# Kernel tuning notes

Hardware: AMD Instinct MI355X
Metric: run time of the kernel (lower is better)

The kernel has to match this reference:

```python
import jax, jax.numpy as jnp
import numpy as np

N, E = 50000, 1600000
D_IN, D_HID, D_OUT = 256, 256, 128  # 2*output_dim = 256, output_dim = 128


def glorot(key, shape):
    fan_in, fan_out = shape
    limit = np.sqrt(6.0 / (fan_in + fan_out)).astype(np.float32)
    return jax.random.uniform(key, shape, jnp.float32, -limit, limit)


def setup_inputs() -> dict:
    key = jax.random.key(0)
    k0, k1, k2, k3 = jax.random.split(key, 4)
    x = jax.random.normal(k0, (N, D_IN), jnp.float32)
    edge_index = jax.random.randint(k1, (2, E), 0, N, jnp.int32)
    W1 = glorot(k2, (D_IN, D_HID))
    b1 = jnp.zeros((D_HID,), jnp.float32)
    W2 = glorot(k3, (D_HID, D_OUT))
    b2 = jnp.zeros((D_OUT,), jnp.float32)
    return {"x": x, "edge_index": edge_index, "W1": W1, "b1": b1, "W2": W2, "b2": b2}


def gcn_propagate(x, src, dst, num_nodes):
    """One hop of D^-1/2 (A + I) D^-1/2 @ x (PyG gcn_norm with self-loops)."""
    loops = jnp.arange(num_nodes, dtype=src.dtype)
    src_sl = jnp.concatenate([src, loops])  # [E + N]
    dst_sl = jnp.concatenate([dst, loops])
    ones = jnp.ones(src_sl.shape, x.dtype)
    deg = jax.ops.segment_sum(ones, dst_sl, num_segments=num_nodes)  # >= 1 (self-loop)
    dinv = jax.lax.rsqrt(jnp.maximum(deg, 1e-12))
    norm = dinv[src_sl] * dinv[dst_sl]  # [E + N]
    msgs = x[src_sl] * norm[:, None]    # gather + scale, [E+N, D]
    return jax.ops.segment_sum(msgs, dst_sl, num_segments=num_nodes)


def reference(x, edge_index, W1, b1, W2, b2):
    src, dst = edge_index[0], edge_index[1]
    n = x.shape[0]
    # SGConv(K=1): propagate then linear. conv1 + ReLU
    h = jax.nn.relu(gcn_propagate(x, src, dst, n) @ W1 + b1)
    # conv2 (GAE branch)
    return gcn_propagate(h, src, dst, n) @ W2 + b2
```

## Files before the change

### kernel.cpp

```cpp
#include <hip/hip_runtime.h>

typedef short s16x8 __attribute__((ext_vector_type(8)));
typedef float f32x4 __attribute__((ext_vector_type(4)));
typedef float f32x2 __attribute__((ext_vector_type(2)));

#define TILE 2048

__device__ __forceinline__ unsigned int brne(float f) {
    unsigned int u = __float_as_uint(f);
    return (u + 0x7FFFu + ((u >> 16) & 1u)) >> 16;
}
__device__ __forceinline__ float blo(unsigned int u) { return __uint_as_float(u << 16); }
__device__ __forceinline__ float bhi(unsigned int u) { return __uint_as_float(u & 0xFFFF0000u); }

__device__ __forceinline__ unsigned int pk_bf16(float lo, float hi) {
    unsigned int r;
    asm("v_cvt_pk_bf16_f32 %0, %1, %2" : "=v"(r) : "v"(lo), "v"(hi));
    return r;
}

__device__ __forceinline__ void acc8p(f32x2* a, const uint4 u, const f32x2 w2) {
    a[0] += (f32x2){blo(u.x), bhi(u.x)} * w2;
    a[1] += (f32x2){blo(u.y), bhi(u.y)} * w2;
    a[2] += (f32x2){blo(u.z), bhi(u.z)} * w2;
    a[3] += (f32x2){blo(u.w), bhi(u.w)} * w2;
}

__device__ __forceinline__ void acc16p(f32x2* a, const uint4 u, const f32x2 w2) {
    a[0] += __builtin_amdgcn_cvt_pk_f32_fp8((int)u.x, false) * w2;
    a[1] += __builtin_amdgcn_cvt_pk_f32_fp8((int)u.x, true)  * w2;
    a[2] += __builtin_amdgcn_cvt_pk_f32_fp8((int)u.y, false) * w2;
    a[3] += __builtin_amdgcn_cvt_pk_f32_fp8((int)u.y, true)  * w2;
    a[4] += __builtin_amdgcn_cvt_pk_f32_fp8((int)u.z, false) * w2;
    a[5] += __builtin_amdgcn_cvt_pk_f32_fp8((int)u.z, true)  * w2;
    a[6] += __builtin_amdgcn_cvt_pk_f32_fp8((int)u.w, false) * w2;
    a[7] += __builtin_amdgcn_cvt_pk_f32_fp8((int)u.w, true)  * w2;
}


__global__ void k_bhist_tw(const int* __restrict__ dst, int* __restrict__ bucket_cnt,
                           int e, int nb, int nbt,
                           const float* __restrict__ W1, const float* __restrict__ W2,
                           unsigned short* __restrict__ W1t, unsigned short* __restrict__ W2t) {
    const int tid = threadIdx.x;
    if ((int)blockIdx.x >= nbt) {
        const int t = ((int)blockIdx.x - nbt) * 256 + tid;
        if (t < 65536) {
            const int k = t >> 8, nn = t & 255;
            W1t[nn * 256 + k] = (unsigned short)brne(W1[t]);
        } else {
            const int u = t - 65536;
            const int k = u >> 7, nn = u & 127;
            W2t[nn * 256 + k] = (unsigned short)brne(W2[u]);
        }
        return;
    }
    __shared__ int h[256];
    h[tid] = 0;
    __syncthreads();
    const int base = blockIdx.x * TILE + tid;
#pragma unroll
    for (int k = 0; k < 8; k++) {
        const int i = base + k * 256;
        if (i < e) atomicAdd(&h[dst[i] >> 8], 1);
    }
    __syncthreads();
    if (tid < nb && h[tid]) atomicAdd(&bucket_cnt[tid], h[tid]);
}

__global__ void k_bscan(const int* __restrict__ bucket_cnt, int* __restrict__ bucket_base,
                        int* __restrict__ bucket_cursor, int nb, int e) {
    __shared__ int sh[256];
    const int tid = threadIdx.x;
    const int v = (tid < nb) ? bucket_cnt[tid] : 0;
    int x = v;
    sh[tid] = x;
    __syncthreads();
    for (int off = 1; off < 256; off <<= 1) {
        const int t = (tid >= off) ? sh[tid - off] : 0;
        __syncthreads();
        if (tid >= off) { x += t; sh[tid] = x; }
        __syncthreads();
    }
    if (tid < nb) { bucket_base[tid] = x - v; bucket_cursor[tid] = x - v; }
    if (tid == 0) bucket_base[nb] = e;
}

__global__ void k_bscatter(const int* __restrict__ src, const int* __restrict__ dst,
                           int* __restrict__ bucket_cursor, uint2* __restrict__ eb, int e) {
    __shared__ int h[256], hbase[256], h2[256];
    const int tid = threadIdx.x;
    h[tid] = 0; h2[tid] = 0;
    __syncthreads();
    const int base = blockIdx.x * TILE + tid;
    int s[8], d[8], b[8];
    bool val[8];
#pragma unroll
    for (int k = 0; k < 8; k++) {
        const int i = base + k * 256;
        val[k] = i < e;
        if (val[k]) {
            s[k] = src[i]; d[k] = dst[i]; b[k] = d[k] >> 8;
            atomicAdd(&h[b[k]], 1);
        }
    }
    __syncthreads();
    if (h[tid]) hbase[tid] = atomicAdd(&bucket_cursor[tid], h[tid]);
    __syncthreads();
#pragma unroll
    for (int k = 0; k < 8; k++) {
        if (val[k]) {
            const int off = atomicAdd(&h2[b[k]], 1);
            eb[hbase[b[k]] + off] = make_uint2((unsigned)s[k], (unsigned)d[k]);
        }
    }
}

__global__ void k_nhist_scan(const uint2* __restrict__ eb, const int* __restrict__ bucket_base,
                             int* __restrict__ rowptr, int* __restrict__ part,
                             float* __restrict__ dinv, int n) {
    __shared__ int c[256], sh[256];
    const int tid = threadIdx.x, b = blockIdx.x;
    c[tid] = 0;
    __syncthreads();
    const int beg = bucket_base[b], end = bucket_base[b + 1];
    for (int i = beg + tid; i < end; i += 256)
        atomicAdd(&c[eb[i].y & 255], 1);
    __syncthreads();
    const int v = c[tid];
    const int node = b * 256 + tid;
    if (node < n) dinv[node] = rsqrtf((float)(v + 1));
    int x = v;
    sh[tid] = x;
    __syncthreads();
    for (int off = 1; off < 256; off <<= 1) {
        const int t = (tid >= off) ? sh[tid - off] : 0;
        __syncthreads();
        if (tid >= off) { x += t; sh[tid] = x; }
        __syncthreads();
    }
    if (node <= n) rowptr[node] = x - v;
    if (tid == 255) part[b] = x;
}

template <bool PREW>
__global__ void k_place(const uint2* __restrict__ eb, const int* __restrict__ bucket_base,
                        int* __restrict__ rowptr, const int* __restrict__ part,
                        void* __restrict__ esv, const float* __restrict__ dinv,
                        int n, int nb) {
    __shared__ int sh[256], rp[256], offs[256];
    __shared__ float sdv[256];
    const int tid = threadIdx.x, b = blockIdx.x;
    int x = (tid < nb) ? part[tid] : 0;
    sh[tid] = x;
    __syncthreads();
    for (int off = 1; off < 256; off <<= 1) {
        const int t = (tid >= off) ? sh[tid - off] : 0;
        __syncthreads();
        if (tid >= off) { x += t; sh[tid] = x; }
        __syncthreads();
    }
    const int prefix = (b > 0) ? sh[b - 1] : 0;
    const int node = b * 256 + tid;
    int rg = 0;
    if (node <= n) {
        rg = rowptr[node] + prefix;
        rowptr[node] = rg;
    }
    rp[tid] = rg;
    offs[tid] = 0;
    if (PREW) sdv[tid] = (node < n) ? dinv[node] : 0.f;
    __syncthreads();
    const int beg = bucket_base[b], end = bucket_base[b + 1];
    if (PREW) {
        int2* es2 = (int2*)esv;
        for (int i = beg + tid; i < end; i += 256) {
            const uint2 ed = eb[i];
            const int sI = (int)ed.x, d = (int)ed.y & 255;
            const float w = dinv[sI] * sdv[d];
            const int local = atomicAdd(&offs[d], 1);
            es2[rp[d] + local] = make_int2(sI, __float_as_int(w));
        }
    } else {
        int* es1 = (int*)esv;
        for (int i = beg + tid; i < end; i += 256) {
            const uint2 ed = eb[i];
            const int d = (int)ed.y & 255;
            const int local = atomicAdd(&offs[d], 1);
            es1[rp[d] + local] = (int)ed.x;
        }
    }
}

#define LP 40
template <bool AF32, bool FP8OUT>
__global__ __launch_bounds__(256) void k_gemm(const void* __restrict__ Av,
                                              const unsigned short* __restrict__ Bt,
                                              void* __restrict__ Cout,
                                              int M, int Nc) {
    __shared__ unsigned short As[128 * LP];
    __shared__ unsigned short Bs[128 * LP];

    const int tid = threadIdx.x;
    const int wave = tid >> 6, lane = tid & 63;
    const int wm = (wave >> 1) * 64, wn = (wave & 1) * 64;
    const int l15 = lane & 15, quad = lane >> 4;
    const int mBase = blockIdx.x * 128, nBase = blockIdx.y * 128;

    f32x4 acc[4][4];
#pragma unroll
    for (int i = 0; i < 4; i++)
#pragma unroll
        for (int j = 0; j < 4; j++) acc[i][j] = (f32x4){0.f, 0.f, 0.f, 0.f};

    const int r0 = tid >> 2, kc0 = tid & 3;
    int am0 = mBase + r0;      if (am0 >= M) am0 = M - 1;
    int am1 = mBase + r0 + 64; if (am1 >= M) am1 = M - 1;

    const uint4* Ap0; const uint4* Ap1; const float4* Af0; const float4* Af1;
    if (AF32) {
        Af0 = (const float4*)Av + (size_t)am0 * 64 + kc0 * 2;
        Af1 = (const float4*)Av + (size_t)am1 * 64 + kc0 * 2;
    } else {
        Ap0 = (const uint4*)Av + (size_t)am0 * 32 + kc0;
        Ap1 = (const uint4*)Av + (size_t)am1 * 32 + kc0;
    }
    const uint4* Bp0 = (const uint4*)Bt + (size_t)(nBase + r0) * 32 + kc0;
    const uint4* Bp1 = (const uint4*)Bt + (size_t)(nBase + r0 + 64) * 32 + kc0;

    for (int kt = 0; kt < 8; ++kt) {
        uint4 a0, a1;
        if (AF32) {
            const float4 l0 = Af0[kt * 8], h0 = Af0[kt * 8 + 1];
            const float4 l1 = Af1[kt * 8], h1 = Af1[kt * 8 + 1];
            a0.x = pk_bf16(l0.x, l0.y); a0.y = pk_bf16(l0.z, l0.w);
            a0.z = pk_bf16(h0.x, h0.y); a0.w = pk_bf16(h0.z, h0.w);
            a1.x = pk_bf16(l1.x, l1.y); a1.y = pk_bf16(l1.z, l1.w);
            a1.z = pk_bf16(h1.x, h1.y); a1.w = pk_bf16(h1.z, h1.w);
        } else {
            a0 = Ap0[kt * 4];
            a1 = Ap1[kt * 4];
        }
        const uint4 b0 = Bp0[kt * 4];
        const uint4 b1 = Bp1[kt * 4];
        __syncthreads();
        *(uint4*)&As[r0 * LP + kc0 * 8] = a0;
        *(uint4*)&As[(r0 + 64) * LP + kc0 * 8] = a1;
        *(uint4*)&Bs[r0 * LP + kc0 * 8] = b0;
        *(uint4*)&Bs[(r0 + 64) * LP + kc0 * 8] = b1;
        __syncthreads();

        s16x8 af[4], bf[4];
#pragma unroll
        for (int i = 0; i < 4; i++)
            af[i] = *(const s16x8*)&As[(wm + i * 16 + l15) * LP + quad * 8];
#pragma unroll
        for (int j = 0; j < 4; j++)
            bf[j] = *(const s16x8*)&Bs[(wn + j * 16 + l15) * LP + quad * 8];
#pragma unroll
        for (int i = 0; i < 4; i++)
#pragma unroll
            for (int j = 0; j < 4; j++)
                acc[i][j] = __builtin_amdgcn_mfma_f32_16x16x32_bf16(af[i], bf[j], acc[i][j], 0, 0, 0);
    }

#pragma unroll
    for (int i = 0; i < 4; i++) {
        const int rowb = mBase + wm + i * 16 + quad * 4;
#pragma unroll
        for (int j = 0; j < 4; j++) {
            const int col = nBase + wn + j * 16 + l15;
#pragma unroll
            for (int r = 0; r < 4; r += 2) {
                if (FP8OUT) {
                    const unsigned int pk = __builtin_amdgcn_cvt_pk_fp8_f32(
                        acc[i][j][r], acc[i][j][r + 1], 0, false);
                    if (rowb + r < M)
                        ((unsigned char*)Cout)[(size_t)(rowb + r) * Nc + col] =
                            (unsigned char)pk;
                    if (rowb + r + 1 < M)
                        ((unsigned char*)Cout)[(size_t)(rowb + r + 1) * Nc + col] =
                            (unsigned char)(pk >> 8);
                } else {
                    const unsigned int pk = pk_bf16(acc[i][j][r], acc[i][j][r + 1]);
                    if (rowb + r < M)
                        ((unsigned short*)Cout)[(size_t)(rowb + r) * Nc + col] =
                            (unsigned short)pk;
                    if (rowb + r + 1 < M)
                        ((unsigned short*)Cout)[(size_t)(rowb + r + 1) * Nc + col] =
                            (unsigned short)(pk >> 16);
                }
            }
        }
    }
}


template <bool PREW>
__global__ void k_prop256f8(const uint4* __restrict__ X4,
                            const int* __restrict__ rowptr,
                            const void* __restrict__ esv,
                            const float* __restrict__ dinv,
                            const float* __restrict__ bias,
                            uint4* __restrict__ Y4, int n) {
    const int wid = (int)((blockIdx.x * blockDim.x + threadIdx.x) >> 6);
    const int lane = threadIdx.x & 63;
    const int quad = lane >> 4, l16 = lane & 15;
    if (wid >= n) return;
    const float dd = dinv[wid];
    const int2* es2 = (const int2*)esv;
    const int*  es1 = (const int*)esv;
    f32x2 a[8];
#pragma unroll
    for (int k = 0; k < 8; k++) a[k] = (f32x2){0.f, 0.f};

    const int beg = rowptr[wid], end = rowptr[wid + 1];
    int j = beg + quad;

    auto EDGE = [&](int jj, int& s, float& w) {
        const bool v = jj < end;
        const int idx = v ? jj : 0;
        if (PREW) {
            const int2 p = es2[idx];
            s = p.x;
            w = v ? __int_as_float(p.y) : 0.f;
        } else {
            s = es1[idx];
            w = v ? dinv[s] * dd : 0.f;
        }
    };

    int s0, s1, s2, s3;
    float w0, w1, w2, w3;
    EDGE(j, s0, w0); EDGE(j + 4, s1, w1); EDGE(j + 8, s2, w2); EDGE(j + 12, s3, w3);

    if (quad == 0) {
        const uint4 v = X4[(size_t)wid * 16 + l16];
        acc16p(a, v, (f32x2){dd * dd, dd * dd});
    }

    while (j + 12 < end) {
        const uint4 u0 = X4[(size_t)s0 * 16 + l16];
        const uint4 u1 = X4[(size_t)s1 * 16 + l16];
        const uint4 u2 = X4[(size_t)s2 * 16 + l16];
        const uint4 u3 = X4[(size_t)s3 * 16 + l16];
        j += 16;
        int t0, t1, t2, t3;
        float x0, x1, x2, x3;
        EDGE(j, t0, x0); EDGE(j + 4, t1, x1); EDGE(j + 8, t2, x2); EDGE(j + 12, t3, x3);
        acc16p(a, u0, (f32x2){w0, w0});
        acc16p(a, u1, (f32x2){w1, w1});
        acc16p(a, u2, (f32x2){w2, w2});
        acc16p(a, u3, (f32x2){w3, w3});
        s0 = t0; s1 = t1; s2 = t2; s3 = t3;
        w0 = x0; w1 = x1; w2 = x2; w3 = x3;
    }
    {
        const uint4 u0 = X4[(size_t)s0 * 16 + l16];
        const uint4 u1 = X4[(size_t)s1 * 16 + l16];
        const uint4 u2 = X4[(size_t)s2 * 16 + l16];
        acc16p(a, u0, (f32x2){w0, w0});
        acc16p(a, u1, (f32x2){w1, w1});
        acc16p(a, u2, (f32x2){w2, w2});
    }
#pragma unroll
    for (int k = 0; k < 8; k++) {
        a[k][0] += __shfl_xor(a[k][0], 16);
        a[k][1] += __shfl_xor(a[k][1], 16);
        a[k][0] += __shfl_xor(a[k][0], 32);
        a[k][1] += __shfl_xor(a[k][1], 32);
    }
    if (quad == 0) {
        const float4* bp = (const float4*)bias + l16 * 4;
#pragma unroll
        for (int q = 0; q < 4; q++) {
            const float4 b = bp[q];
            a[2 * q][0]     = fmaxf(a[2 * q][0] + b.x, 0.f);
            a[2 * q][1]     = fmaxf(a[2 * q][1] + b.y, 0.f);
            a[2 * q + 1][0] = fmaxf(a[2 * q + 1][0] + b.z, 0.f);
            a[2 * q + 1][1] = fmaxf(a[2 * q + 1][1] + b.w, 0.f);
        }
        uint4 p0, p1;
        p0.x = pk_bf16(a[0][0], a[0][1]);
        p0.y = pk_bf16(a[1][0], a[1][1]);
        p0.z = pk_bf16(a[2][0], a[2][1]);
        p0.w = pk_bf16(a[3][0], a[3][1]);
        p1.x = pk_bf16(a[4][0], a[4][1]);
        p1.y = pk_bf16(a[5][0], a[5][1]);
        p1.z = pk_bf16(a[6][0], a[6][1]);
        p1.w = pk_bf16(a[7][0], a[7][1]);
        Y4[(size_t)wid * 32 + l16 * 2] = p0;
        Y4[(size_t)wid * 32 + l16 * 2 + 1] = p1;
    }
}

template <bool PREW>
__global__ void k_prop128b(const uint4* __restrict__ X4,
                           const int* __restrict__ rowptr,
                           const void* __restrict__ esv,
                           const float* __restrict__ dinv,
                           const float* __restrict__ bias,
                           float* __restrict__ Yout, int n) {
    const int wid = (int)((blockIdx.x * blockDim.x + threadIdx.x) >> 6);
    const int lane = threadIdx.x & 63;
    const int quad = lane >> 4, l16 = lane & 15;
    if (wid >= n) return;
    const float dd = dinv[wid];
    const int2* es2 = (const int2*)esv;
    const int*  es1 = (const int*)esv;
    f32x2 a[4];
#pragma unroll
    for (int k = 0; k < 4; k++) a[k] = (f32x2){0.f, 0.f};

    const int beg = rowptr[wid], end = rowptr[wid + 1];
    int j = beg + quad;

    auto EDGE = [&](int jj, int& s, float& w) {
        const bool v = jj < end;
        const int idx = v ? jj : 0;
        if (PREW) {
            const int2 p = es2[idx];
            s = p.x;
            w = v ? __int_as_float(p.y) : 0.f;
        } else {
            s = es1[idx];
            w = v ? dinv[s] * dd : 0.f;
        }
    };

    int s0, s1, s2, s3;
    float w0, w1, w2, w3;
    EDGE(j, s0, w0); EDGE(j + 4, s1, w1); EDGE(j + 8, s2, w2); EDGE(j + 12, s3, w3);

    if (quad == 0) {
        const uint4 v = X4[(size_t)wid * 16 + l16];
        acc8p(a, v, (f32x2){dd * dd, dd * dd});
    }

    while (j + 12 < end) {
        const uint4 u0 = X4[(size_t)s0 * 16 + l16];
        const uint4 u1 = X4[(size_t)s1 * 16 + l16];
        const uint4 u2 = X4[(size_t)s2 * 16 + l16];
        const uint4 u3 = X4[(size_t)s3 * 16 + l16];
        j += 16;
        int t0, t1, t2, t3;
        float x0, x1, x2, x3;
        EDGE(j, t0, x0); EDGE(j + 4, t1, x1); EDGE(j + 8, t2, x2); EDGE(j + 12, t3, x3);
        acc8p(a, u0, (f32x2){w0, w0});
        acc8p(a, u1, (f32x2){w1, w1});
        acc8p(a, u2, (f32x2){w2, w2});
        acc8p(a, u3, (f32x2){w3, w3});
        s0 = t0; s1 = t1; s2 = t2; s3 = t3;
        w0 = x0; w1 = x1; w2 = x2; w3 = x3;
    }
    {
        const uint4 u0 = X4[(size_t)s0 * 16 + l16];
        const uint4 u1 = X4[(size_t)s1 * 16 + l16];
        const uint4 u2 = X4[(size_t)s2 * 16 + l16];
        acc8p(a, u0, (f32x2){w0, w0});
        acc8p(a, u1, (f32x2){w1, w1});
        acc8p(a, u2, (f32x2){w2, w2});
    }
#pragma unroll
    for (int k = 0; k < 4; k++) {
        a[k][0] += __shfl_xor(a[k][0], 16);
        a[k][1] += __shfl_xor(a[k][1], 16);
        a[k][0] += __shfl_xor(a[k][0], 32);
        a[k][1] += __shfl_xor(a[k][1], 32);
    }
    if (quad == 0) {
        const float4 b0 = ((const float4*)bias)[l16 * 2];
        const float4 b1 = ((const float4*)bias)[l16 * 2 + 1];
        float4* op = (float4*)Yout + (size_t)wid * 32 + l16 * 2;
        op[0] = make_float4(a[0][0] + b0.x, a[0][1] + b0.y, a[1][0] + b0.z, a[1][1] + b0.w);
        op[1] = make_float4(a[2][0] + b1.x, a[2][1] + b1.y, a[3][0] + b1.z, a[3][1] + b1.w);
    }
}

extern "C" void kernel_launch(void* const* d_in, const int* in_sizes, int n_in,
                              void* d_out, int out_size, void* d_ws, size_t ws_size,
                              hipStream_t stream) {
    const float* x  = (const float*)d_in[0];
    const int*   ei = (const int*)d_in[1];
    const float* W1 = (const float*)d_in[2];
    const float* b1 = (const float*)d_in[3];
    const float* W2 = (const float*)d_in[4];
    const float* b2 = (const float*)d_in[5];
    float* out = (float*)d_out;

    const int n = in_sizes[0] / 256;
    const int e = in_sizes[1] / 2;
    const int* src = ei;
    const int* dst = ei + e;
    const int nb = (n + 255) >> 8;

    auto al = [](size_t v) { return (v + 511) & ~(size_t)511; };
    const size_t fixed = al(sizeof(float) * n) + al(sizeof(int) * (n + 1)) +
                         al(1024) + al(1024) + al(sizeof(int) * 257) + al(1024) +
                         al(2ull * 256 * 256) + al(2ull * 128 * 256) +
                         al((size_t)n * 256) + al(2ull * n * 256) + al(2ull * n * 128);
    const bool prew = (fixed + al(8ull * (size_t)e)) <= ws_size;

    char* wsp = (char*)d_ws;
    size_t off = 0;
    auto alloc = [&](size_t bytes) -> char* {
        char* p = wsp + off;
        off += (bytes + 511) & ~(size_t)511;
        return p;
    };
    float* dinv    = (float*)alloc(sizeof(float) * n);
    int*   rowptr  = (int*)alloc(sizeof(int) * (n + 1));
    int*   part    = (int*)alloc(1024);
    int*   bcnt    = (int*)alloc(1024);
    int*   bbase   = (int*)alloc(sizeof(int) * 257);
    int*   bcur    = (int*)alloc(1024);
    void*  es      = (void*)alloc((prew ? 8ull : 4ull) * (size_t)e);
    unsigned short* W1t = (unsigned short*)alloc(2ull * 256 * 256);
    unsigned short* W2t = (unsigned short*)alloc(2ull * 128 * 256);
    unsigned char*  T1  = (unsigned char*)alloc((size_t)n * 256);
    unsigned short* H   = (unsigned short*)alloc(2ull * n * 256);
    unsigned short* T2  = (unsigned short*)alloc(2ull * n * 128);
    uint2* eb = (uint2*)H;

    const int nb_t = (e + TILE - 1) / TILE;
    const int tw_b = (65536 + 32768) / 256;

    (void)hipMemsetAsync(bcnt, 0, sizeof(int) * 256, stream);
    k_bhist_tw<<<nb_t + tw_b, 256, 0, stream>>>(dst, bcnt, e, nb, nb_t, W1, W2, W1t, W2t);
    k_bscan<<<1, 256, 0, stream>>>(bcnt, bbase, bcur, nb, e);
    k_bscatter<<<nb_t, 256, 0, stream>>>(src, dst, bcur, eb, e);
    k_nhist_scan<<<nb, 256, 0, stream>>>(eb, bbase, rowptr, part, dinv, n);
    if (prew)
        k_place<true><<<nb, 256, 0, stream>>>(eb, bbase, rowptr, part, es, dinv, n, nb);
    else
        k_place<false><<<nb, 256, 0, stream>>>(eb, bbase, rowptr, part, es, dinv, n, nb);

    dim3 g1((n + 127) / 128, 2);
    k_gemm<true, true><<<g1, 256, 0, stream>>>(x, W1t, T1, n, 256);
    if (prew)
        k_prop256f8<true><<<(n + 3) / 4, 256, 0, stream>>>((const uint4*)T1, rowptr, es,
                                                           dinv, b1, (uint4*)H, n);
    else
        k_prop256f8<false><<<(n + 3) / 4, 256, 0, stream>>>((const uint4*)T1, rowptr, es,
                                                            dinv, b1, (uint4*)H, n);

    dim3 g2((n + 127) / 128, 1);
    k_gemm<false, false><<<g2, 256, 0, stream>>>(H, W2t, T2, n, 128);
    if (prew)
        k_prop128b<true><<<(n + 3) / 4, 256, 0, stream>>>((const uint4*)T2, rowptr, es,
                                                          dinv, b2, out, n);
    else
        k_prop128b<false><<<(n + 3) / 4, 256, 0, stream>>>((const uint4*)T2, rowptr, es,
                                                           dinv, b2, out, n);
}
```

Before: 317.1 us.

## Overlap first GEMM with graph preprocessing on a second stream, double-buffer GEMM LDS

The weight transpose and first GEMM are moved to a separate non-blocking stream, joined by events, so they run concurrently with the edge bucketing and CSR build. The bucket scan kernel is folded into the scatter kernel: every block recomputes the prefix sum from the counts, which removes one launch. The GEMM gains a double-buffered shared-memory tile so the next K-slice's global loads overlap the MFMA work on the current one. The cost is doubled LDS per GEMM block, redundant scans in every scatter block, and reliance on static stream and event state.

```diff
diff --git a/kernel.cpp b/kernel.cpp
--- a/kernel.cpp
+++ b/kernel.cpp
@@ -38,24 +38,10 @@
 }
 
 
-__global__ void k_bhist_tw(const int* __restrict__ dst, int* __restrict__ bucket_cnt,
-                           int e, int nb, int nbt,
-                           const float* __restrict__ W1, const float* __restrict__ W2,
-                           unsigned short* __restrict__ W1t, unsigned short* __restrict__ W2t) {
+__global__ void k_bhist(const int* __restrict__ dst, int* __restrict__ bucket_cnt,
+                        int e, int nb) {
+    __shared__ int h[256];
     const int tid = threadIdx.x;
-    if ((int)blockIdx.x >= nbt) {
-        const int t = ((int)blockIdx.x - nbt) * 256 + tid;
-        if (t < 65536) {
-            const int k = t >> 8, nn = t & 255;
-            W1t[nn * 256 + k] = (unsigned short)brne(W1[t]);
-        } else {
-            const int u = t - 65536;
-            const int k = u >> 7, nn = u & 127;
-            W2t[nn * 256 + k] = (unsigned short)brne(W2[u]);
-        }
-        return;
-    }
-    __shared__ int h[256];
     h[tid] = 0;
     __syncthreads();
     const int base = blockIdx.x * TILE + tid;
@@ -68,11 +54,12 @@
     if (tid < nb && h[tid]) atomicAdd(&bucket_cnt[tid], h[tid]);
 }
 
-__global__ void k_bscan(const int* __restrict__ bucket_cnt, int* __restrict__ bucket_base,
-                        int* __restrict__ bucket_cursor, int nb, int e) {
-    __shared__ int sh[256];
+__global__ void k_bscatter(const int* __restrict__ src, const int* __restrict__ dst,
+                           const int* __restrict__ bcnt, int* __restrict__ bbase,
+                           int* __restrict__ bcur, uint2* __restrict__ eb, int e, int nb) {
+    __shared__ int sh[256], sbase[256], h[256], hbase[256], h2[256];
     const int tid = threadIdx.x;
-    const int v = (tid < nb) ? bucket_cnt[tid] : 0;
+    const int v = (tid < nb) ? bcnt[tid] : 0;
     int x = v;
     sh[tid] = x;
     __syncthreads();
@@ -82,14 +69,11 @@
         if (tid >= off) { x += t; sh[tid] = x; }
         __syncthreads();
     }
-    if (tid < nb) { bucket_base[tid] = x - v; bucket_cursor[tid] = x - v; }
-    if (tid == 0) bucket_base[nb] = e;
-}
-
-__global__ void k_bscatter(const int* __restrict__ src, const int* __restrict__ dst,
-                           int* __restrict__ bucket_cursor, uint2* __restrict__ eb, int e) {
-    __shared__ int h[256], hbase[256], h2[256];
-    const int tid = threadIdx.x;
+    sbase[tid] = x - v;
+    if (blockIdx.x == 0) {
+        if (tid < nb) bbase[tid] = x - v;
+        if (tid == 0) bbase[nb] = e;
+    }
     h[tid] = 0; h2[tid] = 0;
     __syncthreads();
     const int base = blockIdx.x * TILE + tid;
@@ -105,7 +89,7 @@
         }
     }
     __syncthreads();
-    if (h[tid]) hbase[tid] = atomicAdd(&bucket_cursor[tid], h[tid]);
+    if (h[tid]) hbase[tid] = sbase[tid] + atomicAdd(&bcur[tid], h[tid]);
     __syncthreads();
 #pragma unroll
     for (int k = 0; k < 8; k++) {
@@ -192,14 +176,27 @@
     }
 }
 
+__global__ void k_tW2(const float* __restrict__ W1, const float* __restrict__ W2,
+                      unsigned short* __restrict__ W1t, unsigned short* __restrict__ W2t) {
+    const int t = blockIdx.x * 256 + threadIdx.x;
+    if (t < 65536) {
+        const int k = t >> 8, nn = t & 255;
+        W1t[nn * 256 + k] = (unsigned short)brne(W1[t]);
+    } else {
+        const int u = t - 65536;
+        const int k = u >> 7, nn = u & 127;
+        W2t[nn * 256 + k] = (unsigned short)brne(W2[u]);
+    }
+}
+
 #define LP 40
 template <bool AF32, bool FP8OUT>
 __global__ __launch_bounds__(256) void k_gemm(const void* __restrict__ Av,
                                               const unsigned short* __restrict__ Bt,
                                               void* __restrict__ Cout,
                                               int M, int Nc) {
-    __shared__ unsigned short As[128 * LP];
-    __shared__ unsigned short Bs[128 * LP];
+    __shared__ unsigned short As[2][128 * LP];
+    __shared__ unsigned short Bs[2][128 * LP];
 
     const int tid = threadIdx.x;
     const int wave = tid >> 6, lane = tid & 63;
@@ -228,8 +225,8 @@
     const uint4* Bp0 = (const uint4*)Bt + (size_t)(nBase + r0) * 32 + kc0;
     const uint4* Bp1 = (const uint4*)Bt + (size_t)(nBase + r0 + 64) * 32 + kc0;
 
-    for (int kt = 0; kt < 8; ++kt) {
-        uint4 a0, a1;
+    uint4 a0, a1, b0, b1;
+    auto LOAD = [&](int kt) {
         if (AF32) {
             const float4 l0 = Af0[kt * 8], h0 = Af0[kt * 8 + 1];
             const float4 l1 = Af1[kt * 8], h1 = Af1[kt * 8 + 1];
@@ -241,27 +238,36 @@
             a0 = Ap0[kt * 4];
             a1 = Ap1[kt * 4];
         }
-        const uint4 b0 = Bp0[kt * 4];
-        const uint4 b1 = Bp1[kt * 4];
-        __syncthreads();
-        *(uint4*)&As[r0 * LP + kc0 * 8] = a0;
-        *(uint4*)&As[(r0 + 64) * LP + kc0 * 8] = a1;
-        *(uint4*)&Bs[r0 * LP + kc0 * 8] = b0;
-        *(uint4*)&Bs[(r0 + 64) * LP + kc0 * 8] = b1;
-        __syncthreads();
-
+        b0 = Bp0[kt * 4];
+        b1 = Bp1[kt * 4];
+    };
+    auto STORE = [&](int buf) {
+        *(uint4*)&As[buf][r0 * LP + kc0 * 8] = a0;
+        *(uint4*)&As[buf][(r0 + 64) * LP + kc0 * 8] = a1;
+        *(uint4*)&Bs[buf][r0 * LP + kc0 * 8] = b0;
+        *(uint4*)&Bs[buf][(r0 + 64) * LP + kc0 * 8] = b1;
+    };
+
+    LOAD(0);
+    STORE(0);
+    __syncthreads();
+    for (int kt = 0; kt < 8; ++kt) {
+        const int cur = kt & 1;
+        if (kt < 7) LOAD(kt + 1);
         s16x8 af[4], bf[4];
 #pragma unroll
         for (int i = 0; i < 4; i++)
-            af[i] = *(const s16x8*)&As[(wm + i * 16 + l15) * LP + quad * 8];
+            af[i] = *(const s16x8*)&As[cur][(wm + i * 16 + l15) * LP + quad * 8];
 #pragma unroll
         for (int j = 0; j < 4; j++)
-            bf[j] = *(const s16x8*)&Bs[(wn + j * 16 + l15) * LP + quad * 8];
+            bf[j] = *(const s16x8*)&Bs[cur][(wn + j * 16 + l15) * LP + quad * 8];
+        if (kt < 7) STORE(cur ^ 1);
 #pragma unroll
         for (int i = 0; i < 4; i++)
 #pragma unroll
             for (int j = 0; j < 4; j++)
                 acc[i][j] = __builtin_amdgcn_mfma_f32_16x16x32_bf16(af[i], bf[j], acc[i][j], 0, 0, 0);
+        __syncthreads();
     }
 
 #pragma unroll
@@ -496,7 +502,7 @@
 
     auto al = [](size_t v) { return (v + 511) & ~(size_t)511; };
     const size_t fixed = al(sizeof(float) * n) + al(sizeof(int) * (n + 1)) +
-                         al(1024) + al(1024) + al(sizeof(int) * 257) + al(1024) +
+                         al(1024) + al(2048) + al(sizeof(int) * 257) +
                          al(2ull * 256 * 256) + al(2ull * 128 * 256) +
                          al((size_t)n * 256) + al(2ull * n * 256) + al(2ull * n * 128);
     const bool prew = (fixed + al(8ull * (size_t)e)) <= ws_size;
@@ -511,9 +517,10 @@
     float* dinv    = (float*)alloc(sizeof(float) * n);
     int*   rowptr  = (int*)alloc(sizeof(int) * (n + 1));
     int*   part    = (int*)alloc(1024);
-    int*   bcnt    = (int*)alloc(1024);
+    int*   bcc     = (int*)alloc(2048);
+    int*   bcnt    = bcc;
+    int*   bcur    = bcc + 256;
     int*   bbase   = (int*)alloc(sizeof(int) * 257);
-    int*   bcur    = (int*)alloc(1024);
     void*  es      = (void*)alloc((prew ? 8ull : 4ull) * (size_t)e);
     unsigned short* W1t = (unsigned short*)alloc(2ull * 256 * 256);
     unsigned short* W2t = (unsigned short*)alloc(2ull * 128 * 256);
@@ -523,20 +530,40 @@
     uint2* eb = (uint2*)H;
 
     const int nb_t = (e + TILE - 1) / TILE;
-    const int tw_b = (65536 + 32768) / 256;
-
-    (void)hipMemsetAsync(bcnt, 0, sizeof(int) * 256, stream);
-    k_bhist_tw<<<nb_t + tw_b, 256, 0, stream>>>(dst, bcnt, e, nb, nb_t, W1, W2, W1t, W2t);
-    k_bscan<<<1, 256, 0, stream>>>(bcnt, bbase, bcur, nb, e);
-    k_bscatter<<<nb_t, 256, 0, stream>>>(src, dst, bcur, eb, e);
+
+    static hipStream_t sB = nullptr;
+    static hipEvent_t evF = nullptr, evW = nullptr;
+    static int inited = 0;
+    if (!inited) {
+        inited = 1;
+        if (hipStreamCreateWithFlags(&sB, hipStreamNonBlocking) != hipSuccess) sB = nullptr;
+        if (hipEventCreateWithFlags(&evF, hipEventDisableTiming) != hipSuccess) evF = nullptr;
+        if (hipEventCreateWithFlags(&evW, hipEventDisableTiming) != hipSuccess) evW = nullptr;
+    }
+    const bool par = (sB != nullptr) && (evF != nullptr) && (evW != nullptr);
+    hipStream_t gs = par ? sB : stream;
+
+    if (par) {
+        (void)hipEventRecord(evF, stream);
+        (void)hipStreamWaitEvent(sB, evF, 0);
+    }
+
+    k_tW2<<<(65536 + 32768) / 256, 256, 0, gs>>>(W1, W2, W1t, W2t);
+    dim3 g1((n + 127) / 128, 2);
+    k_gemm<true, true><<<g1, 256, 0, gs>>>(x, W1t, T1, n, 256);
+    if (par) (void)hipEventRecord(evW, gs);
+
+    (void)hipMemsetAsync(bcc, 0, 2048, stream);
+    k_bhist<<<nb_t, 256, 0, stream>>>(dst, bcnt, e, nb);
+    k_bscatter<<<nb_t, 256, 0, stream>>>(src, dst, bcnt, bbase, bcur, eb, e, nb);
     k_nhist_scan<<<nb, 256, 0, stream>>>(eb, bbase, rowptr, part, dinv, n);
     if (prew)
         k_place<true><<<nb, 256, 0, stream>>>(eb, bbase, rowptr, part, es, dinv, n, nb);
     else
         k_place<false><<<nb, 256, 0, stream>>>(eb, bbase, rowptr, part, es, dinv, n, nb);
 
-    dim3 g1((n + 127) / 128, 2);
-    k_gemm<true, true><<<g1, 256, 0, stream>>>(x, W1t, T1, n, 256);
+    if (par) (void)hipStreamWaitEvent(stream, evW, 0);
+
     if (prew)
         k_prop256f8<true><<<(n + 3) / 4, 256, 0, stream>>>((const uint4*)T1, rowptr, es,
                                                            dinv, b1, (uint4*)H, n);
```

Result: slower. 349.2 us (+10.1%).
